# Kernel tuning notes

Hardware: AMD Instinct MI355X
Metric: run time of the kernel (lower is better)

The kernel has to match this reference:

```python
import jax, jax.numpy as jnp
import numpy as np

B, P, ENC_DIM = 256, 196, 2048
WORD_DIM, ATT_DIM = 512, 512

def setup_inputs() -> dict:
    key = jax.random.key(0)
    ks = jax.random.split(key, 8)
    s_enc = 1.0 / np.sqrt(ENC_DIM)
    s_dec = 1.0 / np.sqrt(WORD_DIM)
    s_fin = 1.0 / np.sqrt(ATT_DIM)
    return {
        "encoder_out": jax.random.normal(ks[0], (B, P, ENC_DIM), dtype=jnp.float32),
        "decoder_out": jax.random.normal(ks[1], (B, WORD_DIM), dtype=jnp.float32),
        "W_enc": jax.random.uniform(ks[2], (ENC_DIM, ATT_DIM), jnp.float32, -s_enc, s_enc),
        "b_enc": jax.random.uniform(ks[3], (ATT_DIM,), jnp.float32, -s_enc, s_enc),
        "W_dec": jax.random.uniform(ks[4], (WORD_DIM, ATT_DIM), jnp.float32, -s_dec, s_dec),
        "b_dec": jax.random.uniform(ks[5], (ATT_DIM,), jnp.float32, -s_dec, s_dec),
        "W_fin": jax.random.uniform(ks[6], (ATT_DIM,), jnp.float32, -s_fin, s_fin),
        "b_fin": jax.random.uniform(ks[7], (), jnp.float32, -s_fin, s_fin),
    }

def reference(encoder_out, decoder_out, W_enc, b_enc, W_dec, b_dec, W_fin, b_fin):
    # encoder projection: [B, P, A]
    att_enc = jnp.einsum('bpe,ea->bpa', encoder_out, W_enc) + b_enc
    # decoder projection: [B, A]
    att_dec = decoder_out @ W_dec + b_dec
    # additive combine + relu + final scalar projection -> [B, P]
    hidden = jax.nn.relu(att_enc + att_dec[:, None, :])
    att = jnp.einsum('bpa,a->bp', hidden, W_fin) + b_fin
    # softmax over pixels (dim=1)
    att_weights = jax.nn.softmax(att, axis=1)
    # weighted sum of encoder features -> [B, ENC_DIM]
    return jnp.einsum('bpe,bp->be', encoder_out, att_weights)
```

## Files before the change

### kernel.cpp

```cpp
#include <hip/hip_runtime.h>

#define B_   256
#define P_   196
#define E_   2048
#define WD_  512
#define A_   512
#define M_   (B_ * P_)

typedef __bf16 bf16x8 __attribute__((ext_vector_type(8)));
typedef float  f32x4  __attribute__((ext_vector_type(4)));

using u16 = unsigned short;
using u32 = unsigned int;

__device__ inline u16 f2bf(float f) {
    u32 u; __builtin_memcpy(&u, &f, 4);
    u += 0x7FFFu + ((u >> 16) & 1u); return (u16)(u >> 16);
}

__device__ inline void gld_lds16(const void* g, void* l) {
    __builtin_amdgcn_global_load_lds(
        (const __attribute__((address_space(1))) u32*)g,
        (__attribute__((address_space(3))) u32*)l, 16, 0, 0);
}

__global__ __launch_bounds__(256) void k_prep(const float* __restrict__ We,
                                              u16* __restrict__ Wt) {
    __shared__ float tile[32][33];
    const int tx = threadIdx.x & 31, ty = threadIdx.x >> 5;
    const int k0 = blockIdx.x * 32, n0 = blockIdx.y * 32;
#pragma unroll
    for (int i = 0; i < 4; ++i)
        tile[ty + i * 8][tx] = We[(size_t)(k0 + ty + i * 8) * A_ + n0 + tx];
    __syncthreads();
#pragma unroll
    for (int i = 0; i < 4; ++i)
        Wt[(size_t)(n0 + ty + i * 8) * E_ + k0 + tx] = f2bf(tile[tx][ty + i * 8]);
}

__global__ __launch_bounds__(512) void k_att_dec(const float* __restrict__ dec,
                                                 const float* __restrict__ Wd,
                                                 const float* __restrict__ bd,
                                                 float* __restrict__ att_dec) {
    int b = blockIdx.x, a = threadIdx.x;
    __shared__ float sd[WD_];
    sd[a] = dec[b * WD_ + a];
    __syncthreads();
    float acc = bd[a];
#pragma unroll 8
    for (int e = 0; e < WD_; ++e)
        acc = fmaf(sd[e], Wd[e * A_ + a], acc);
    att_dec[b * A_ + a] = acc;
}

__global__ __launch_bounds__(512, 4) void k_logits(
        const float* __restrict__ enc, const u16* __restrict__ Wt,
        const float* __restrict__ be, const float* __restrict__ Wf,
        const float* __restrict__ att_dec, float* __restrict__ att) {
    __shared__ u16    sB[2][A_ * 32];
    __shared__ bf16x8 sA[2][256];
    __shared__ float  sred[8][64];

    const int t   = threadIdx.x;
    const int w   = t >> 6;
    const int L   = t & 63;
    const int l15 = L & 15;
    const int q   = L >> 4;
    const int m0  = blockIdx.x * 64;

    const f32x4 zero = {0.f, 0.f, 0.f, 0.f};
    f32x4 acc[4][4];
#pragma unroll
    for (int rt = 0; rt < 4; ++rt)
#pragma unroll
        for (int ct = 0; ct < 4; ++ct) acc[rt][ct] = zero;

    const int s    = t >> 1, h = t & 1;
    const int srt  = s >> 6;
    const int sL   = s & 63;
    const float* ap = enc + (size_t)(m0 + srt * 16 + (sL & 15)) * E_
                          + (sL >> 4) * 8 + h * 4;
    u32* slds  = (u32*)&sA[0][s] + h * 2;
    u32* slds1 = (u32*)&sA[1][s] + h * 2;

    const int brow  = L >> 2;
    const int bslot = (L & 3) ^ ((L >> 3) & 3);
    const u16* bsrc = Wt + (size_t)(w * 64 + brow) * E_ + bslot * 8;
    u16* bdst0 = &sB[0][(w * 64) * 32];
    u16* bdst1 = &sB[1][(w * 64) * 32];

    int bro[4];
#pragma unroll
    for (int ct = 0; ct < 4; ++ct) {
        int n = w * 64 + ct * 16 + l15;
        int slot = q ^ ((l15 >> 1) & 3);
        bro[ct] = n * 32 + slot * 8;
    }

#pragma unroll
    for (int j = 0; j < 4; ++j)
        gld_lds16(bsrc + (size_t)j * 16 * E_, bdst0 + j * 512);
    float4 aN1 = *(const float4*)(ap);
    float4 aN2 = *(const float4*)(ap + 32);
    {
        u32 lo = (u32)f2bf(aN1.x) | ((u32)f2bf(aN1.y) << 16);
        u32 hi = (u32)f2bf(aN1.z) | ((u32)f2bf(aN1.w) << 16);
        slds[0] = lo; slds[1] = hi;
    }
    aN1 = aN2;
    __syncthreads();

    for (int kt = 0; kt < 64; ++kt) {
        const int buf = kt & 1;

        if (kt < 63) {
            const u16* bs = bsrc + (size_t)(kt + 1) * 32;
            u16* bd = buf ? bdst0 : bdst1;
#pragma unroll
            for (int j = 0; j < 4; ++j)
                gld_lds16(bs + (size_t)j * 16 * E_, bd + j * 512);
        }
        const int kA = (kt + 2 < 64) ? kt + 2 : 63;
        aN2 = *(const float4*)(ap + (size_t)kA * 32);

        bf16x8 af[4];
#pragma unroll
        for (int rt = 0; rt < 4; ++rt) af[rt] = sA[buf][rt * 64 + L];
        const u16* sbb = sB[buf];
        bf16x8 bv[4];
#pragma unroll
        for (int ct = 0; ct < 4; ++ct)
            __builtin_memcpy(&bv[ct], sbb + bro[ct], 16);

#pragma unroll
        for (int ct = 0; ct < 4; ++ct) {
#pragma unroll
            for (int rt = 0; rt < 4; ++rt)
                acc[rt][ct] = __builtin_amdgcn_mfma_f32_16x16x32_bf16(
                    af[rt], bv[ct], acc[rt][ct], 0, 0, 0);
        }

        {
            u32 lo = (u32)f2bf(aN1.x) | ((u32)f2bf(aN1.y) << 16);
            u32 hi = (u32)f2bf(aN1.z) | ((u32)f2bf(aN1.w) << 16);
            u32* d = buf ? slds : slds1;
            d[0] = lo; d[1] = hi;
        }
        aN1 = aN2;

        __syncthreads();
    }

    float wf[4], bev[4];
#pragma unroll
    for (int ct = 0; ct < 4; ++ct) {
        int n = w * 64 + ct * 16 + l15;
        wf[ct]  = Wf[n];
        bev[ct] = be[n];
    }
#pragma unroll
    for (int rt = 0; rt < 4; ++rt) {
#pragma unroll
        for (int reg = 0; reg < 4; ++reg) {
            int ml = rt * 16 + q * 4 + reg;
            int b  = (m0 + ml) / P_;
            const float* adp = att_dec + (size_t)b * A_ + w * 64 + l15;
            float p = 0.f;
#pragma unroll
            for (int ct = 0; ct < 4; ++ct) {
                float hx = acc[rt][ct][reg] + bev[ct] + adp[ct * 16];
                p = fmaf(fmaxf(hx, 0.f), wf[ct], p);
            }
#pragma unroll
            for (int off = 8; off > 0; off >>= 1)
                p += __shfl_down(p, off, 16);
            if (l15 == 0) sred[w][ml] = p;
        }
    }
    __syncthreads();
    if (t < 64) {
        float r = 0.f;
#pragma unroll
        for (int ww = 0; ww < 8; ++ww) r += sred[ww][t];
        att[m0 + t] = r;
    }
}

__global__ __launch_bounds__(256) void k_out(const float* __restrict__ enc,
                                             const float* __restrict__ att,
                                             float* __restrict__ out) {
    int b = blockIdx.x, t = threadIdx.x;
    __shared__ float sw[P_];
    __shared__ float red[8];
    __shared__ f32x4 spart[4][64];

    float v = (t < P_) ? att[b * P_ + t] : -1e30f;
    float m = v;
#pragma unroll
    for (int off = 32; off > 0; off >>= 1)
        m = fmaxf(m, __shfl_down(m, off, 64));
    int wid = t >> 6;
    if ((t & 63) == 0) red[wid] = m;
    __syncthreads();
    m = fmaxf(fmaxf(red[0], red[1]), fmaxf(red[2], red[3]));

    float ev = (t < P_) ? __expf(v - m) : 0.f;
    float ssum = ev;
#pragma unroll
    for (int off = 32; off > 0; off >>= 1)
        ssum += __shfl_down(ssum, off, 64);
    if ((t & 63) == 0) red[4 + wid] = ssum;
    __syncthreads();
    ssum = red[4] + red[5] + red[6] + red[7];
    if (t < P_) sw[t] = ev / ssum;
    __syncthreads();

    const int tq = t >> 6, lane = t & 63;
    const int e0 = blockIdx.y * 256 + lane * 4;
    const float* ep = enc + (size_t)b * P_ * E_ + e0;
    f32x4 acc = {0.f, 0.f, 0.f, 0.f};
    const int p0 = tq * 49;
#pragma unroll 7
    for (int i = 0; i < 49; ++i) {
        int p = p0 + i;
        float4 qv = *(const float4*)(ep + (size_t)p * E_);
        float wgt = sw[p];
        acc[0] = fmaf(wgt, qv.x, acc[0]);
        acc[1] = fmaf(wgt, qv.y, acc[1]);
        acc[2] = fmaf(wgt, qv.z, acc[2]);
        acc[3] = fmaf(wgt, qv.w, acc[3]);
    }
    spart[tq][lane] = acc;
    __syncthreads();
    if (tq == 0) {
        f32x4 r = spart[0][lane];
#pragma unroll
        for (int g = 1; g < 4; ++g) {
            f32x4 x = spart[g][lane];
            r[0] += x[0]; r[1] += x[1]; r[2] += x[2]; r[3] += x[3];
        }
        float* op = out + (size_t)b * E_ + e0;
        op[0] = r[0]; op[1] = r[1]; op[2] = r[2]; op[3] = r[3];
    }
}

extern "C" void kernel_launch(void* const* d_in, const int* in_sizes, int n_in,
                              void* d_out, int out_size, void* d_ws, size_t ws_size,
                              hipStream_t stream) {
    const float* enc   = (const float*)d_in[0];
    const float* dec   = (const float*)d_in[1];
    const float* W_enc = (const float*)d_in[2];
    const float* b_enc = (const float*)d_in[3];
    const float* W_dec = (const float*)d_in[4];
    const float* b_dec = (const float*)d_in[5];
    const float* W_fin = (const float*)d_in[6];

    float* att_dec = (float*)d_ws;
    float* att     = att_dec + B_ * A_;
    u16*   Wt      = (u16*)(att + M_);

    k_prep<<<dim3(E_ / 32, A_ / 32), 256, 0, stream>>>(W_enc, Wt);
    k_att_dec<<<B_, 512, 0, stream>>>(dec, W_dec, b_dec, att_dec);
    k_logits<<<M_ / 64, 512, 0, stream>>>(enc, Wt, b_enc, W_fin, att_dec, att);
    k_out<<<dim3(B_, 8), 256, 0, stream>>>(enc, att, (float*)d_out);
}
```

Baseline: 804.4 us.

## Deepen GEMM prefetch and replace full-drain syncs with partial vmcnt waits

The encoder-tile prefetch in the logits GEMM loop now runs three k-steps ahead instead of two. Each `__syncthreads` that drained all outstanding global loads is replaced by an explicit `s_waitcnt vmcnt(6)` plus an LDS-only wait and a raw barrier, so global loads for later steps stay in flight across iterations. The loop is also unrolled by two so buffer indices become compile-time constants. This depends on correct hand-counted load ordering and uses one extra float4 register set per thread.

Measured after the change: 811.8 us. About the same (+0.9%).

```diff
diff --git a/kernel.cpp b/kernel.cpp
--- a/kernel.cpp
+++ b/kernel.cpp
@@ -100,56 +100,62 @@
 #pragma unroll
     for (int j = 0; j < 4; ++j)
         gld_lds16(bsrc + (size_t)j * 16 * E_, bdst0 + j * 512);
-    float4 aN1 = *(const float4*)(ap);
-    float4 aN2 = *(const float4*)(ap + 32);
+    asm volatile("" ::: "memory");
+    float4 aN1, aN2, aN3;
     {
-        u32 lo = (u32)f2bf(aN1.x) | ((u32)f2bf(aN1.y) << 16);
-        u32 hi = (u32)f2bf(aN1.z) | ((u32)f2bf(aN1.w) << 16);
+        float4 a0 = *(const float4*)(ap);
+        aN1 = *(const float4*)(ap + 32);
+        aN2 = *(const float4*)(ap + 64);
+        u32 lo = (u32)f2bf(a0.x) | ((u32)f2bf(a0.y) << 16);
+        u32 hi = (u32)f2bf(a0.z) | ((u32)f2bf(a0.w) << 16);
         slds[0] = lo; slds[1] = hi;
     }
-    aN1 = aN2;
-    __syncthreads();
-
-    for (int kt = 0; kt < 64; ++kt) {
-        const int buf = kt & 1;
-
-        if (kt < 63) {
-            const u16* bs = bsrc + (size_t)(kt + 1) * 32;
-            u16* bd = buf ? bdst0 : bdst1;
-#pragma unroll
-            for (int j = 0; j < 4; ++j)
-                gld_lds16(bs + (size_t)j * 16 * E_, bd + j * 512);
-        }
-        const int kA = (kt + 2 < 64) ? kt + 2 : 63;
-        aN2 = *(const float4*)(ap + (size_t)kA * 32);
-
-        bf16x8 af[4];
-#pragma unroll
-        for (int rt = 0; rt < 4; ++rt) af[rt] = sA[buf][rt * 64 + L];
-        const u16* sbb = sB[buf];
-        bf16x8 bv[4];
-#pragma unroll
-        for (int ct = 0; ct < 4; ++ct)
-            __builtin_memcpy(&bv[ct], sbb + bro[ct], 16);
-
-#pragma unroll
-        for (int ct = 0; ct < 4; ++ct) {
-#pragma unroll
-            for (int rt = 0; rt < 4; ++rt)
-                acc[rt][ct] = __builtin_amdgcn_mfma_f32_16x16x32_bf16(
-                    af[rt], bv[ct], acc[rt][ct], 0, 0, 0);
-        }
-
-        {
-            u32 lo = (u32)f2bf(aN1.x) | ((u32)f2bf(aN1.y) << 16);
-            u32 hi = (u32)f2bf(aN1.z) | ((u32)f2bf(aN1.w) << 16);
-            u32* d = buf ? slds : slds1;
-            d[0] = lo; d[1] = hi;
-        }
-        aN1 = aN2;
-
-        __syncthreads();
-    }
+    asm volatile("s_waitcnt lgkmcnt(0)" ::: "memory");
+    __builtin_amdgcn_s_barrier();
+
+#define KSTEP(KT, BUF)                                                        \
+  {                                                                           \
+    const int knx_ = ((KT) + 1 < 64) ? (KT) + 1 : 63;                         \
+    const u16* bs_ = bsrc + (size_t)knx_ * 32;                                \
+    u16* bd_ = (BUF) ? bdst0 : bdst1;                                         \
+    _Pragma("unroll")                                                         \
+    for (int j = 0; j < 4; ++j)                                               \
+        gld_lds16(bs_ + (size_t)j * 16 * E_, bd_ + j * 512);                  \
+    asm volatile("" ::: "memory");        \
+    const int kA_ = ((KT) + 3 < 64) ? (KT) + 3 : 63;                          \
+    aN3 = *(const float4*)(ap + (size_t)kA_ * 32);                            \
+    asm volatile("s_waitcnt vmcnt(6)" ::: "memory");                          \
+    bf16x8 af_[4];                                                            \
+    _Pragma("unroll")                                                         \
+    for (int rt = 0; rt < 4; ++rt) af_[rt] = sA[BUF][rt * 64 + L];            \
+    bf16x8 bv_[4];                                                            \
+    _Pragma("unroll")                                                         \
+    for (int ct = 0; ct < 4; ++ct)                                            \
+        __builtin_memcpy(&bv_[ct], &sB[BUF][0] + bro[ct], 16);                \
+    _Pragma("unroll")                                                         \
+    for (int ct = 0; ct < 4; ++ct) {                                          \
+        _Pragma("unroll")                                                     \
+        for (int rt = 0; rt < 4; ++rt)                                        \
+            acc[rt][ct] = __builtin_amdgcn_mfma_f32_16x16x32_bf16(            \
+                af_[rt], bv_[ct], acc[rt][ct], 0, 0, 0);                      \
+    }                                                                         \
+    {                                                                         \
+        u32 lo = (u32)f2bf(aN1.x) | ((u32)f2bf(aN1.y) << 16);                 \
+        u32 hi = (u32)f2bf(aN1.z) | ((u32)f2bf(aN1.w) << 16);                 \
+        u32* d_ = (BUF) ? slds : slds1;       \
+        d_[0] = lo; d_[1] = hi;                                               \
+    }                                                                         \
+    aN1 = aN2; aN2 = aN3;                                                     \
+    asm volatile("s_waitcnt lgkmcnt(0)" ::: "memory");                        \
+    __builtin_amdgcn_s_barrier();                                             \
+  }
+
+#pragma unroll 1
+    for (int kt = 0; kt < 64; kt += 2) {
+        KSTEP(kt, 0)
+        KSTEP(kt + 1, 1)
+    }
+#undef KSTEP
 
     float wf[4], bev[4];
 #pragma unroll
```
